# Kernel tuning notes

Measured on AMD Instinct MI355X. Metric: run time of the kernel, lower is better.

## Reference

```python
import jax, jax.numpy as jnp
import numpy as np

NUM_QUBITS = 4
SHOTS = 1000
BATCH = 8192
IN_SIZE = 4096
OUT_SIZE = 4096


def setup_inputs() -> dict:
    key = jax.random.key(0)
    k_x, k_w, k_b, k_q = jax.random.split(key, 4)
    x = jax.random.normal(k_x, (BATCH, IN_SIZE), dtype=jnp.float32)
    W = jax.random.normal(k_w, (OUT_SIZE, IN_SIZE), dtype=jnp.float32) * (1.0 / np.sqrt(IN_SIZE))
    b = jax.random.normal(k_b, (OUT_SIZE,), dtype=jnp.float32) * 0.01
    # Each shot's measurement outcome: num_qubits independent uniform bits
    # == one uniform integer in [0, 2**num_qubits).
    quantum_outcomes = jax.random.randint(k_q, (BATCH, SHOTS), 0, 2 ** NUM_QUBITS, dtype=jnp.int32)
    return {"x": x, "W": W, "b": b, "quantum_outcomes": quantum_outcomes}


def reference(x, W, b, quantum_outcomes):
    # classical path: nn.Linear
    classical = jnp.einsum("bi,oi->bo", x, W) + b  # [B, OUT]
    # normalized by max outcome, broadcast across the output dim.
    max_outcome = float(2 ** NUM_QUBITS - 1)
    expectation = jnp.mean(quantum_outcomes.astype(jnp.float32), axis=1) / max_outcome  # [B]
    return classical + expectation[:, None]
```

## Files before the change

kernel.cpp:

```cpp
#include <hip/hip_runtime.h>
#include <hip/hip_bf16.h>

typedef __attribute__((ext_vector_type(8))) short short8;
typedef __attribute__((ext_vector_type(4))) float f32x4;
typedef unsigned short ushort_t;


__device__ __forceinline__ ushort_t f2bf_rne(float f) {
    unsigned u = __float_as_uint(f);
    u += 0x7FFF + ((u >> 16) & 1);
    return (ushort_t)(u >> 16);
}

__device__ __forceinline__ unsigned pack2(float lo, float hi) {
    unsigned a = __float_as_uint(lo);
    a += 0x7FFF + ((a >> 16) & 1);
    unsigned b = __float_as_uint(hi);
    b += 0x7FFF + ((b >> 16) & 1);
    return (a >> 16) | (b & 0xFFFF0000u);
}

__device__ __forceinline__ short8 pack8(float4 a, float4 b) {
    short8 r;
    r[0] = (short)f2bf_rne(a.x); r[1] = (short)f2bf_rne(a.y);
    r[2] = (short)f2bf_rne(a.z); r[3] = (short)f2bf_rne(a.w);
    r[4] = (short)f2bf_rne(b.x); r[5] = (short)f2bf_rne(b.y);
    r[6] = (short)f2bf_rne(b.z); r[7] = (short)f2bf_rne(b.w);
    return r;
}

__global__ void conv_kernel(const float* __restrict__ src, ushort_t* __restrict__ dst) {
    long long base = (long long)blockIdx.x * 1024;
    const float4* s4 = (const float4*)src;
    uint2* d2 = (uint2*)dst;
    #pragma unroll
    for (int c = 0; c < 4; c++) {
        long long idx = base + c * 256 + threadIdx.x;
        float4 a = s4[idx];
        uint2 r;
        r.x = pack2(a.x, a.y);
        r.y = pack2(a.z, a.w);
        d2[idx] = r;
    }
}

__global__ void expect_kernel(const int* __restrict__ q, float* __restrict__ e,
                              int rows, int shots) {
    int row = blockIdx.x * (blockDim.x >> 6) + (threadIdx.x >> 6);
    int lane = threadIdx.x & 63;
    if (row >= rows) return;
    const int4* rp4 = (const int4*)(q + (long long)row * shots);
    int nvec = shots >> 2;
    int s = 0;
    for (int j = lane; j < nvec; j += 64) {
        int4 v = rp4[j];
        s += v.x + v.y + v.z + v.w;
    }
    #pragma unroll
    for (int off = 32; off; off >>= 1) s += __shfl_down(s, off, 64);
    if (lane == 0) e[row] = (float)s * (1.0f / (1000.0f * 15.0f));
}


#define GLDS(srcp, dstp) \
    __builtin_amdgcn_global_load_lds( \
        (const __attribute__((address_space(1))) unsigned int*)(srcp), \
        (__attribute__((address_space(3))) unsigned int*)(dstp), 16, 0, 0)

#define BAR() do { asm volatile("" ::: "memory"); \
                   __builtin_amdgcn_s_barrier(); \
                   asm volatile("" ::: "memory"); } while (0)

#define VMCNT(n) asm volatile("s_waitcnt vmcnt(" #n ")" ::: "memory")

#define PH_READ_A(kh) do { \
    const ushort_t* At = As + ((b * 2 + (kh)) << 13); \
    _Pragma("unroll") \
    for (int i = 0; i < 8; i++) af[i] = *(const short8*)(At + rdA0 + (i << 9)); \
} while (0)

#define PH_READ_B(kh, nh) do { \
    const ushort_t* Bt = Bs + ((b * 2 + (kh)) << 13); \
    bfr[0] = *(const short8*)(Bt + rdB0 + ((nh) << 10)); \
    bfr[1] = *(const short8*)(Bt + rdB0 + ((nh) << 10) + 512); \
} while (0)

#define PH_MFMA(nh) do { \
    __builtin_amdgcn_s_setprio(1); \
    _Pragma("unroll") \
    for (int i = 0; i < 8; i++) { \
        acc[i][(nh) * 2]     = __builtin_amdgcn_mfma_f32_16x16x32_bf16(af[i], bfr[0], acc[i][(nh) * 2], 0, 0, 0); \
        acc[i][(nh) * 2 + 1] = __builtin_amdgcn_mfma_f32_16x16x32_bf16(af[i], bfr[1], acc[i][(nh) * 2 + 1], 0, 0, 0); \
    } \
    __builtin_amdgcn_s_setprio(0); \
} while (0)

__global__ __launch_bounds__(512, 2)
void gemm8_kernel(const ushort_t* __restrict__ A, const ushort_t* __restrict__ B,
                  const float* __restrict__ bias, const float* __restrict__ expect,
                  float* __restrict__ C, int M, int N, int K) {
    __shared__ ushort_t As[2 * 2 * 256 * 32];
    __shared__ ushort_t Bs[2 * 2 * 256 * 32];

    const int pid = blockIdx.x;
    const int xcd = pid & 7;
    const int p   = pid >> 3;
    const int pid_n = xcd * 2 + (p & 1);
    const int pid_m = p >> 1;

    const int tid  = threadIdx.x;
    const int lane = tid & 63;
    const int wave = tid >> 6;
    const int wr = wave >> 2;
    const int wc = wave & 3;
    const int quad = lane >> 4;
    const int l15  = lane & 15;

    const int rslot = (quad ^ ((l15 >> 1) & 3)) * 8;
    const int rdA0 = (wr * 128 + l15) * 32 + rslot;
    const int rdB0 = (wc * 64 + l15) * 32 + rslot;

    const int srow0 = tid >> 2;
    const int ssl   = tid & 3;
    const int sc    = ssl ^ ((srow0 >> 1) & 3);

    const ushort_t* aS0 = A + ((long long)pid_m * 256 + srow0) * K + sc * 8;
    const ushort_t* aS1 = aS0 + 128LL * K;
    const ushort_t* bS0 = B + ((long long)pid_n * 256 + srow0) * K + sc * 8;
    const ushort_t* bS1 = bS0 + 128LL * K;

    f32x4 acc[8][4];
    #pragma unroll
    for (int i = 0; i < 8; i++)
        #pragma unroll
        for (int j = 0; j < 4; j++)
            acc[i][j] = (f32x4)(0.0f);

    const int NT = K / 64;

    GLDS(aS0,      As + tid * 8);
    GLDS(aS1,      As + tid * 8 + 4096);
    GLDS(bS0,      Bs + tid * 8);
    GLDS(bS1,      Bs + tid * 8 + 4096);
    GLDS(aS0 + 32, As + (1 << 13) + tid * 8);
    GLDS(aS1 + 32, As + (1 << 13) + tid * 8 + 4096);
    GLDS(bS0 + 32, Bs + (1 << 13) + tid * 8);
    GLDS(bS1 + 32, Bs + (1 << 13) + tid * 8 + 4096);
    VMCNT(0);
    BAR();

    short8 af[8], bfr[2];

    for (int t = 0; t < NT - 1; ++t) {
        const int b  = t & 1;
        const int bn = b ^ 1;
        const long long k1 = (long long)(t + 1) * 64;
        ushort_t* An0 = As + ((bn * 2 + 0) << 13) + tid * 8;
        ushort_t* An1 = As + ((bn * 2 + 1) << 13) + tid * 8;
        ushort_t* Bn0 = Bs + ((bn * 2 + 0) << 13) + tid * 8;
        ushort_t* Bn1 = Bs + ((bn * 2 + 1) << 13) + tid * 8;

        PH_READ_A(0);
        PH_READ_B(0, 0);
        GLDS(aS0 + k1, An0);
        GLDS(aS1 + k1, An0 + 4096);
        BAR();
        PH_MFMA(0);
        BAR();

        PH_READ_B(0, 1);
        GLDS(bS0 + k1, Bn0);
        GLDS(bS1 + k1, Bn0 + 4096);
        BAR();
        PH_MFMA(1);
        VMCNT(4);
        BAR();

        PH_READ_A(1);
        PH_READ_B(1, 0);
        GLDS(aS0 + k1 + 32, An1);
        GLDS(aS1 + k1 + 32, An1 + 4096);
        BAR();
        PH_MFMA(0);
        BAR();

        PH_READ_B(1, 1);
        GLDS(bS0 + k1 + 32, Bn1);
        GLDS(bS1 + k1 + 32, Bn1 + 4096);
        BAR();
        PH_MFMA(1);
        VMCNT(4);
        BAR();
    }

    {
        const int b = (NT - 1) & 1;
        PH_READ_A(0);
        PH_READ_B(0, 0);
        BAR();
        PH_MFMA(0);
        BAR();
        PH_READ_B(0, 1);
        BAR();
        PH_MFMA(1);
        VMCNT(0);
        BAR();
        PH_READ_A(1);
        PH_READ_B(1, 0);
        BAR();
        PH_MFMA(0);
        BAR();
        PH_READ_B(1, 1);
        BAR();
        PH_MFMA(1);
    }

    long long row0 = (long long)pid_m * 256 + wr * 128;
    int col0 = pid_n * 256 + wc * 64;
    float bj[4];
    #pragma unroll
    for (int j = 0; j < 4; j++) bj[j] = bias[col0 + j * 16 + l15];
    #pragma unroll
    for (int i = 0; i < 8; i++) {
        #pragma unroll
        for (int rr = 0; rr < 4; rr++) {
            long long row = row0 + i * 16 + quad * 4 + rr;
            float er = expect[row];
            float* Crow = C + row * (long long)N;
            #pragma unroll
            for (int j = 0; j < 4; j++)
                Crow[col0 + j * 16 + l15] = acc[i][j][rr] + bj[j] + er;
        }
    }
}

#define BM 128
#define BN 128
#define BK 64

__global__ __launch_bounds__(256, 2)
void gemm_f32stage_kernel(const float* __restrict__ A, const float* __restrict__ B,
                          const float* __restrict__ bias, const float* __restrict__ expect,
                          float* __restrict__ C, int M, int N, int K) {
    __shared__ ushort_t As[BM * BK];
    __shared__ ushort_t Bs[BN * BK];

    int pid = blockIdx.x;
    const int xcd = pid & 7;
    const int p   = pid >> 3;
    int pid_n = xcd * 4 + (p & 3);
    int pid_m = p >> 2;

    const int tid  = threadIdx.x;
    const int lane = tid & 63;
    const int wave = tid >> 6;
    const int wm = (wave >> 1) * 64;
    const int wn = (wave & 1) * 64;

    const int srow = tid >> 1;
    const int chalf = (tid & 1) * 4;

    const float* a_base = A + ((long long)pid_m * BM + srow) * K + chalf * 8;
    const float* b_base = B + ((long long)pid_n * BN + srow) * K + chalf * 8;

    f32x4 acc[4][4];
    #pragma unroll
    for (int i = 0; i < 4; i++)
        #pragma unroll
        for (int j = 0; j < 4; j++)
            acc[i][j] = (f32x4)(0.0f);

    const int quad = lane >> 4;
    const int l15  = lane & 15;
    const int rlow = l15 & 7;

    for (int k0 = 0; k0 < K; k0 += BK) {
        {
            const float4* ap = (const float4*)(a_base + k0);
            const float4* bp = (const float4*)(b_base + k0);
            float4 fa[8], fb[8];
            #pragma unroll
            for (int c = 0; c < 8; c++) { fa[c] = ap[c]; fb[c] = bp[c]; }
            #pragma unroll
            for (int c = 0; c < 4; c++) {
                int sl = ((chalf + c) ^ (srow & 7)) * 8;
                *(short8*)(As + srow * BK + sl) = pack8(fa[2*c], fa[2*c+1]);
                *(short8*)(Bs + srow * BK + sl) = pack8(fb[2*c], fb[2*c+1]);
            }
        }
        __syncthreads();

        #pragma unroll
        for (int ks = 0; ks < 2; ks++) {
            int q = ks * 4 + quad;
            int sw = (q ^ rlow) * 8;
            short8 af[4], bf[4];
            #pragma unroll
            for (int i = 0; i < 4; i++) {
                af[i] = *(const short8*)(As + (wm + i * 16 + l15) * BK + sw);
                bf[i] = *(const short8*)(Bs + (wn + i * 16 + l15) * BK + sw);
            }
            #pragma unroll
            for (int i = 0; i < 4; i++)
                #pragma unroll
                for (int j = 0; j < 4; j++)
                    acc[i][j] = __builtin_amdgcn_mfma_f32_16x16x32_bf16(
                        af[i], bf[j], acc[i][j], 0, 0, 0);
        }
        __syncthreads();
    }

    long long row0 = (long long)pid_m * BM + wm;
    int col0 = pid_n * BN + wn;
    #pragma unroll
    for (int j = 0; j < 4; j++) {
        int col = col0 + j * 16 + l15;
        float bjv = bias[col];
        #pragma unroll
        for (int i = 0; i < 4; i++) {
            #pragma unroll
            for (int r = 0; r < 4; r++) {
                long long row = row0 + i * 16 + quad * 4 + r;
                C[row * N + col] = acc[i][j][r] + bjv + expect[row];
            }
        }
    }
}

extern "C" void kernel_launch(void* const* d_in, const int* in_sizes, int n_in,
                              void* d_out, int out_size, void* d_ws, size_t ws_size,
                              hipStream_t stream) {
    const float* x = (const float*)d_in[0];
    const float* W = (const float*)d_in[1];
    const float* b = (const float*)d_in[2];
    const int*   q = (const int*)d_in[3];
    float* out = (float*)d_out;

    const int M = 8192, N = 4096, K = 4096, SHOTS = 1000;

    float* expect = (float*)d_ws;
    size_t need = 32768 + (size_t)M * K * 2 + (size_t)N * K * 2;

    if (ws_size >= need) {
        ushort_t* xb = (ushort_t*)((char*)d_ws + 32768);
        ushort_t* wb = xb + (size_t)M * K;
        conv_kernel<<<8192, 256, 0, stream>>>(x, xb);
        conv_kernel<<<4096, 256, 0, stream>>>(W, wb);
        expect_kernel<<<M / 4, 256, 0, stream>>>(q, expect, M, SHOTS);
        gemm8_kernel<<<(M / 256) * (N / 256), 512, 0, stream>>>(xb, wb, b, expect, out, M, N, K);
    } else {
        expect_kernel<<<M / 4, 256, 0, stream>>>(q, expect, M, SHOTS);
        gemm_f32stage_kernel<<<(M / BM) * (N / BN), 256, 0, stream>>>(x, W, b, expect, out, M, N, K);
    }
}
```

Baseline: 517.7 us.

## Restructure GEMM main loop into two barrier phases with 32-MFMA bursts

The per-iteration schedule drops from four LDS-read/MFMA sub-phases with eight barriers to two half-K phases with two barriers. Each phase reads all four B fragments and issues 32 MFMAs back-to-back. All four A prefetches for the next tile are issued at the start of the iteration and all four B prefetches mid-iteration. The vmcnt waits are retuned to match the new load order, including a partial wait in the prologue. This cuts barrier and synchronisation overhead and gives longer MFMA streams, at the cost of two extra fragment registers and less fine-grained interleaving of loads with compute.

```diff
diff --git a/kernel.cpp b/kernel.cpp
--- a/kernel.cpp
+++ b/kernel.cpp
@@ -79,18 +79,21 @@
     for (int i = 0; i < 8; i++) af[i] = *(const short8*)(At + rdA0 + (i << 9)); \
 } while (0)
 
-#define PH_READ_B(kh, nh) do { \
+#define PH_READ_B4(kh) do { \
     const ushort_t* Bt = Bs + ((b * 2 + (kh)) << 13); \
-    bfr[0] = *(const short8*)(Bt + rdB0 + ((nh) << 10)); \
-    bfr[1] = *(const short8*)(Bt + rdB0 + ((nh) << 10) + 512); \
+    bfr[0] = *(const short8*)(Bt + rdB0); \
+    bfr[1] = *(const short8*)(Bt + rdB0 + 512); \
+    bfr[2] = *(const short8*)(Bt + rdB0 + 1024); \
+    bfr[3] = *(const short8*)(Bt + rdB0 + 1536); \
 } while (0)
 
-#define PH_MFMA(nh) do { \
+#define PH_MFMA32() do { \
     __builtin_amdgcn_s_setprio(1); \
     _Pragma("unroll") \
     for (int i = 0; i < 8; i++) { \
-        acc[i][(nh) * 2]     = __builtin_amdgcn_mfma_f32_16x16x32_bf16(af[i], bfr[0], acc[i][(nh) * 2], 0, 0, 0); \
-        acc[i][(nh) * 2 + 1] = __builtin_amdgcn_mfma_f32_16x16x32_bf16(af[i], bfr[1], acc[i][(nh) * 2 + 1], 0, 0, 0); \
+        _Pragma("unroll") \
+        for (int j = 0; j < 4; j++) \
+            acc[i][j] = __builtin_amdgcn_mfma_f32_16x16x32_bf16(af[i], bfr[j], acc[i][j], 0, 0, 0); \
     } \
     __builtin_amdgcn_s_setprio(0); \
 } while (0)
@@ -140,16 +143,16 @@
 
     GLDS(aS0,      As + tid * 8);
     GLDS(aS1,      As + tid * 8 + 4096);
+    GLDS(aS0 + 32, As + (1 << 13) + tid * 8);
+    GLDS(aS1 + 32, As + (1 << 13) + tid * 8 + 4096);
     GLDS(bS0,      Bs + tid * 8);
     GLDS(bS1,      Bs + tid * 8 + 4096);
-    GLDS(aS0 + 32, As + (1 << 13) + tid * 8);
-    GLDS(aS1 + 32, As + (1 << 13) + tid * 8 + 4096);
     GLDS(bS0 + 32, Bs + (1 << 13) + tid * 8);
     GLDS(bS1 + 32, Bs + (1 << 13) + tid * 8 + 4096);
-    VMCNT(0);
+    VMCNT(2);
     BAR();
 
-    short8 af[8], bfr[2];
+    short8 af[8], bfr[4];
 
     for (int t = 0; t < NT - 1; ++t) {
         const int b  = t & 1;
@@ -160,59 +163,37 @@
         ushort_t* Bn0 = Bs + ((bn * 2 + 0) << 13) + tid * 8;
         ushort_t* Bn1 = Bs + ((bn * 2 + 1) << 13) + tid * 8;
 
+        GLDS(aS0 + k1,      An0);
+        GLDS(aS1 + k1,      An0 + 4096);
+        GLDS(aS0 + k1 + 32, An1);
+        GLDS(aS1 + k1 + 32, An1 + 4096);
         PH_READ_A(0);
-        PH_READ_B(0, 0);
-        GLDS(aS0 + k1, An0);
-        GLDS(aS1 + k1, An0 + 4096);
-        BAR();
-        PH_MFMA(0);
-        BAR();
-
-        PH_READ_B(0, 1);
-        GLDS(bS0 + k1, Bn0);
-        GLDS(bS1 + k1, Bn0 + 4096);
-        BAR();
-        PH_MFMA(1);
+        PH_READ_B4(0);
+        PH_MFMA32();
         VMCNT(4);
         BAR();
 
-        PH_READ_A(1);
-        PH_READ_B(1, 0);
-        GLDS(aS0 + k1 + 32, An1);
-        GLDS(aS1 + k1 + 32, An1 + 4096);
-        BAR();
-        PH_MFMA(0);
-        BAR();
-
-        PH_READ_B(1, 1);
+        GLDS(bS0 + k1,      Bn0);
+        GLDS(bS1 + k1,      Bn0 + 4096);
         GLDS(bS0 + k1 + 32, Bn1);
         GLDS(bS1 + k1 + 32, Bn1 + 4096);
-        BAR();
-        PH_MFMA(1);
-        VMCNT(4);
+        PH_READ_A(1);
+        PH_READ_B4(1);
+        PH_MFMA32();
+        VMCNT(2);
         BAR();
     }
 
     {
         const int b = (NT - 1) & 1;
         PH_READ_A(0);
-        PH_READ_B(0, 0);
-        BAR();
-        PH_MFMA(0);
-        BAR();
-        PH_READ_B(0, 1);
-        BAR();
-        PH_MFMA(1);
+        PH_READ_B4(0);
+        PH_MFMA32();
         VMCNT(0);
         BAR();
         PH_READ_A(1);
-        PH_READ_B(1, 0);
-        BAR();
-        PH_MFMA(0);
-        BAR();
-        PH_READ_B(1, 1);
-        BAR();
-        PH_MFMA(1);
+        PH_READ_B4(1);
+        PH_MFMA32();
     }
 
     long long row0 = (long long)pid_m * 256 + wr * 128;
```

Result: slower. 569.7 us (+10.0%).
